# Kernel tuning notes

Measured on AMD Instinct MI355X. Metric: run time of the kernel, lower is better.

## Reference

```python
import jax, jax.numpy as jnp
import numpy as np

B, T, J, D = 32, 1024, 256, 512

def setup_inputs() -> dict:
    key = jax.random.key(0)
    k1, k2, k3 = jax.random.split(key, 3)
    h = jax.random.normal(k1, (B, T, D), dtype=jnp.float32)
    u = jax.random.normal(k2, (B, J, D), dtype=jnp.float32)
    w = jax.random.normal(k3, (1, 3 * D), dtype=jnp.float32) * 0.05
    return {"h": h, "u": u, "w": w}

def reference(h, u, w):
    # S[b,i,j] = w . concat([h_i, u_j, h_i*u_j])
    # Algebraic decomposition: w = [w_h, w_u, w_m]
    d = h.shape[-1]
    w = w[0]
    w_h, w_u, w_m = w[:d], w[d:2*d], w[2*d:]
    # [B,T,1] + [B,1,J] + [B,T,J]
    term_h = jnp.einsum('btd,d->bt', h, w_h)[:, :, None]
    term_u = jnp.einsum('bjd,d->bj', u, w_u)[:, None, :]
    term_m = jnp.einsum('btd,bjd->btj', h * w_m, u)
    return term_h + term_u + term_m
```

## Files before the change

### kernel.cpp

```cpp
#include <hip/hip_runtime.h>
#include <hip/hip_bf16.h>
#include <stdint.h>

#define B_ 32
#define T_ 1024
#define J_ 256
#define D_ 512

typedef __attribute__((ext_vector_type(8))) short short8;
typedef __attribute__((ext_vector_type(4))) float floatx4;

__global__ __launch_bounds__(256) void prep_u_kernel(
    const float* __restrict__ u, const float* __restrict__ w,
    __hip_bfloat16* __restrict__ B2, float* __restrict__ tu)
{
    int row  = blockIdx.x * 4 + (threadIdx.x >> 6);
    int lane = threadIdx.x & 63;
    const float* src = u + (size_t)row * D_;
    int base = lane * 8;

    float4 v0  = *(const float4*)(src + base);
    float4 v1  = *(const float4*)(src + base + 4);
    float4 wh0 = *(const float4*)(w + base);
    float4 wh1 = *(const float4*)(w + base + 4);
    float4 wu0 = *(const float4*)(w + D_ + base);
    float4 wu1 = *(const float4*)(w + D_ + base + 4);
    float4 wm0 = *(const float4*)(w + 2*D_ + base);
    float4 wm1 = *(const float4*)(w + 2*D_ + base + 4);

    float s = v0.x*wu0.x + v0.y*wu0.y + v0.z*wu0.z + v0.w*wu0.w
            + v1.x*wu1.x + v1.y*wu1.y + v1.z*wu1.z + v1.w*wu1.w;

    float vals[8] = {
        v0.x*wm0.x + wh0.x, v0.y*wm0.y + wh0.y,
        v0.z*wm0.z + wh0.z, v0.w*wm0.w + wh0.w,
        v1.x*wm1.x + wh1.x, v1.y*wm1.y + wh1.y,
        v1.z*wm1.z + wh1.z, v1.w*wm1.w + wh1.w };

    union { __hip_bfloat16 b[8]; uint4 q; } pk;
#pragma unroll
    for (int i = 0; i < 8; i++) pk.b[i] = __float2bfloat16(vals[i]);
    *(uint4*)(B2 + (size_t)row * D_ + base) = pk.q;

#pragma unroll
    for (int off = 32; off > 0; off >>= 1) s += __shfl_down(s, off, 64);
    if (lane == 0) tu[row] = s;
}

__device__ inline void gload_lds16(const void* g, void* l) {
    __builtin_amdgcn_global_load_lds(
        (__attribute__((address_space(1))) void*)(g),
        (__attribute__((address_space(3))) void*)(l),
        16, 0, 0);
}

__global__ __launch_bounds__(1024, 4) void gemm_kernel(
    const float* __restrict__ h,
    const __hip_bfloat16* __restrict__ B2,
    const float* __restrict__ tu,
    float* __restrict__ out)
{
    __shared__ __align__(16) __hip_bfloat16 sB[2][256 * 128];

    const int b   = blockIdx.x;
    const int tM  = blockIdx.y;
    const int tid = threadIdx.x;
    const int w = tid >> 6, lane = tid & 63;
    const int wr = w >> 1, wc = w & 1;

    const int fr = lane & 15;
    const int kq = lane >> 4;

    const float* Aw = h + ((size_t)b * T_ + tM * 128 + wr * 16 + fr) * D_ + kq * 8;
    const __hip_bfloat16* Bb = B2 + (size_t)b * J_ * D_;

    floatx4 acc[8];
#pragma unroll
    for (int n = 0; n < 8; n++) acc[n] = (floatx4)0.0f;

#pragma unroll
    for (int i = 0; i < 4; i++) {
        int q = i * 1024 + tid;
        int j = q >> 4;
        int c = (q & 15) ^ (j & 15);
        gload_lds16(Bb + (size_t)j * D_ + c * 8, &sB[0][q * 8]);
    }

    float4 aC0 = *(const float4*)(Aw);
    float4 aC1 = *(const float4*)(Aw + 4);
    float4 aN0, aN1;
    __syncthreads();

    for (int p = 0; p < 4; p++) {
        if (p < 3) {
#pragma unroll
            for (int i = 0; i < 4; i++) {
                int q = i * 1024 + tid;
                int j = q >> 4;
                int c = (q & 15) ^ (j & 15);
                gload_lds16(Bb + (size_t)j * D_ + (p + 1) * 128 + c * 8,
                            &sB[(p + 1) & 1][q * 8]);
            }
        }
        const __hip_bfloat16* sBp = sB[p & 1];

#pragma unroll
        for (int ks = 0; ks < 4; ks++) {
            int ki = p * 4 + ks;
            if (ki < 15) {
                const float* ap = Aw + (ki + 1) * 32;
                aN0 = *(const float4*)(ap);
                aN1 = *(const float4*)(ap + 4);
            }
            union { __hip_bfloat16 e[8]; short8 v; } af;
            af.e[0]=__float2bfloat16(aC0.x); af.e[1]=__float2bfloat16(aC0.y);
            af.e[2]=__float2bfloat16(aC0.z); af.e[3]=__float2bfloat16(aC0.w);
            af.e[4]=__float2bfloat16(aC1.x); af.e[5]=__float2bfloat16(aC1.y);
            af.e[6]=__float2bfloat16(aC1.z); af.e[7]=__float2bfloat16(aC1.w);
#pragma unroll
            for (int n = 0; n < 8; n++) {
                int j = wc * 128 + n * 16 + fr;
                int c = ks * 4 + kq;
                short8 bf = *(const short8*)(sBp + (j * 16 + (c ^ (j & 15))) * 8);
                acc[n] = __builtin_amdgcn_mfma_f32_16x16x32_bf16(
                    af.v, bf, acc[n], 0, 0, 0);
            }
            if (ki < 15) { aC0 = aN0; aC1 = aN1; }
        }
        __syncthreads();
    }

    const size_t outB = (size_t)b * T_ * J_;
    const int r0 = tM * 128 + wr * 16 + kq * 4;
    const float* tub = tu + b * J_;
#pragma unroll
    for (int n = 0; n < 8; n++) {
        int col = wc * 128 + n * 16 + fr;
        float tuv = tub[col];
#pragma unroll
        for (int r = 0; r < 4; r++) {
            out[outB + (size_t)(r0 + r) * J_ + col] = acc[n][r] + tuv;
        }
    }
}

extern "C" void kernel_launch(void* const* d_in, const int* in_sizes, int n_in,
                              void* d_out, int out_size, void* d_ws, size_t ws_size,
                              hipStream_t stream)
{
    const float* h = (const float*)d_in[0];
    const float* u = (const float*)d_in[1];
    const float* w = (const float*)d_in[2];
    float* out = (float*)d_out;

    uint8_t* ws = (uint8_t*)d_ws;
    __hip_bfloat16* B2 = (__hip_bfloat16*)ws;
    float* tu = (float*)(ws + (size_t)B_ * J_ * D_ * 2);

    prep_u_kernel<<<dim3(B_ * J_ / 4), 256, 0, stream>>>(u, w, B2, tu);

    gemm_kernel<<<dim3(B_, T_ / 128), 1024, 0, stream>>>(h, B2, tu, out);
}
```

Baseline: 127.9 us.

## Halve GEMM block tile and K-stage, use finer waitcnt-based barriers

The GEMM kernel now uses 512-thread blocks covering 64 rows of T instead of 128, with K staged in 64-wide LDS chunks over 8 stages. The B swizzle is adjusted to match, and LDS use per block drops to half. The __syncthreads calls are replaced with an explicit s_waitcnt vmcnt(4)/s_barrier, so the in-flight A register prefetches do not block the barrier. The aim is more blocks per CU and better latency hiding, at the cost of more barriers per K and less B reuse per block.

```diff
diff --git a/kernel.cpp b/kernel.cpp
--- a/kernel.cpp
+++ b/kernel.cpp
@@ -54,13 +54,13 @@
         16, 0, 0);
 }
 
-__global__ __launch_bounds__(1024, 4) void gemm_kernel(
+__global__ __launch_bounds__(512, 4) void gemm_kernel(
     const float* __restrict__ h,
     const __hip_bfloat16* __restrict__ B2,
     const float* __restrict__ tu,
     float* __restrict__ out)
 {
-    __shared__ __align__(16) __hip_bfloat16 sB[2][256 * 128];
+    __shared__ __align__(16) __hip_bfloat16 sB[2][256 * 64];
 
     const int b   = blockIdx.x;
     const int tM  = blockIdx.y;
@@ -71,7 +71,7 @@
     const int fr = lane & 15;
     const int kq = lane >> 4;
 
-    const float* Aw = h + ((size_t)b * T_ + tM * 128 + wr * 16 + fr) * D_ + kq * 8;
+    const float* Aw = h + ((size_t)b * T_ + tM * 64 + wr * 16 + fr) * D_ + kq * 8;
     const __hip_bfloat16* Bb = B2 + (size_t)b * J_ * D_;
 
     floatx4 acc[8];
@@ -80,58 +80,80 @@
 
 #pragma unroll
     for (int i = 0; i < 4; i++) {
-        int q = i * 1024 + tid;
-        int j = q >> 4;
-        int c = (q & 15) ^ (j & 15);
+        int q = i * 512 + tid;
+        int j = q >> 3;
+        int c = (q & 7) ^ (j & 7);
         gload_lds16(Bb + (size_t)j * D_ + c * 8, &sB[0][q * 8]);
     }
+    __builtin_amdgcn_sched_barrier(0);
 
-    float4 aC0 = *(const float4*)(Aw);
-    float4 aC1 = *(const float4*)(Aw + 4);
-    float4 aN0, aN1;
-    __syncthreads();
+    float4 aA0 = *(const float4*)(Aw);
+    float4 aA1 = *(const float4*)(Aw + 4);
+    float4 aB0 = *(const float4*)(Aw + 32);
+    float4 aB1 = *(const float4*)(Aw + 36);
 
-    for (int p = 0; p < 4; p++) {
-        if (p < 3) {
+    asm volatile("s_waitcnt vmcnt(4) lgkmcnt(0)\n\ts_barrier" ::: "memory");
+
+    for (int p = 0; p < 8; p++) {
+        if (p < 7) {
 #pragma unroll
             for (int i = 0; i < 4; i++) {
-                int q = i * 1024 + tid;
-                int j = q >> 4;
-                int c = (q & 15) ^ (j & 15);
-                gload_lds16(Bb + (size_t)j * D_ + (p + 1) * 128 + c * 8,
+                int q = i * 512 + tid;
+                int j = q >> 3;
+                int c = (q & 7) ^ (j & 7);
+                gload_lds16(Bb + (size_t)j * D_ + (p + 1) * 64 + c * 8,
                             &sB[(p + 1) & 1][q * 8]);
             }
+            __builtin_amdgcn_sched_barrier(0);
         }
         const __hip_bfloat16* sBp = sB[p & 1];
 
-#pragma unroll
-        for (int ks = 0; ks < 4; ks++) {
-            int ki = p * 4 + ks;
-            if (ki < 15) {
-                const float* ap = Aw + (ki + 1) * 32;
-                aN0 = *(const float4*)(ap);
-                aN1 = *(const float4*)(ap + 4);
+        {
+            union { __hip_bfloat16 e[8]; short8 v; } af;
+            af.e[0]=__float2bfloat16(aA0.x); af.e[1]=__float2bfloat16(aA0.y);
+            af.e[2]=__float2bfloat16(aA0.z); af.e[3]=__float2bfloat16(aA0.w);
+            af.e[4]=__float2bfloat16(aA1.x); af.e[5]=__float2bfloat16(aA1.y);
+            af.e[6]=__float2bfloat16(aA1.z); af.e[7]=__float2bfloat16(aA1.w);
+            if (p < 7) {
+                const float* ap = Aw + (2 * p + 2) * 32;
+                aA0 = *(const float4*)(ap);
+                aA1 = *(const float4*)(ap + 4);
             }
-            union { __hip_bfloat16 e[8]; short8 v; } af;
-            af.e[0]=__float2bfloat16(aC0.x); af.e[1]=__float2bfloat16(aC0.y);
-            af.e[2]=__float2bfloat16(aC0.z); af.e[3]=__float2bfloat16(aC0.w);
-            af.e[4]=__float2bfloat16(aC1.x); af.e[5]=__float2bfloat16(aC1.y);
-            af.e[6]=__float2bfloat16(aC1.z); af.e[7]=__float2bfloat16(aC1.w);
 #pragma unroll
             for (int n = 0; n < 8; n++) {
                 int j = wc * 128 + n * 16 + fr;
-                int c = ks * 4 + kq;
-                short8 bf = *(const short8*)(sBp + (j * 16 + (c ^ (j & 15))) * 8);
+                int cc = kq;
+                short8 bf = *(const short8*)(sBp + (j * 8 + (cc ^ (j & 7))) * 8);
                 acc[n] = __builtin_amdgcn_mfma_f32_16x16x32_bf16(
                     af.v, bf, acc[n], 0, 0, 0);
             }
-            if (ki < 15) { aC0 = aN0; aC1 = aN1; }
         }
-        __syncthreads();
+        {
+            union { __hip_bfloat16 e[8]; short8 v; } af;
+            af.e[0]=__float2bfloat16(aB0.x); af.e[1]=__float2bfloat16(aB0.y);
+            af.e[2]=__float2bfloat16(aB0.z); af.e[3]=__float2bfloat16(aB0.w);
+            af.e[4]=__float2bfloat16(aB1.x); af.e[5]=__float2bfloat16(aB1.y);
+            af.e[6]=__float2bfloat16(aB1.z); af.e[7]=__float2bfloat16(aB1.w);
+            if (p < 7) {
+                const float* ap = Aw + (2 * p + 3) * 32;
+                aB0 = *(const float4*)(ap);
+                aB1 = *(const float4*)(ap + 4);
+            }
+#pragma unroll
+            for (int n = 0; n < 8; n++) {
+                int j = wc * 128 + n * 16 + fr;
+                int cc = 4 + kq;
+                short8 bf = *(const short8*)(sBp + (j * 8 + (cc ^ (j & 7))) * 8);
+                acc[n] = __builtin_amdgcn_mfma_f32_16x16x32_bf16(
+                    af.v, bf, acc[n], 0, 0, 0);
+            }
+        }
+        if (p < 7)
+            asm volatile("s_waitcnt vmcnt(4) lgkmcnt(0)\n\ts_barrier" ::: "memory");
     }
 
     const size_t outB = (size_t)b * T_ * J_;
-    const int r0 = tM * 128 + wr * 16 + kq * 4;
+    const int r0 = tM * 64 + wr * 16 + kq * 4;
     const float* tub = tu + b * J_;
 #pragma unroll
     for (int n = 0; n < 8; n++) {
@@ -159,5 +181,5 @@
 
     prep_u_kernel<<<dim3(B_ * J_ / 4), 256, 0, stream>>>(u, w, B2, tu);
 
-    gemm_kernel<<<dim3(B_, T_ / 128), 1024, 0, stream>>>(h, B2, tu, out);
+    gemm_kernel<<<dim3(B_, T_ / 64), 512, 0, stream>>>(h, B2, tu, out);
 }
```

Result: slower. 131.6 us (+2.9%).
